# Kernel tuning notes

Hardware: AMD Instinct MI355X
Metric: run time of the kernel (lower is better)

Reference implementation:

```python
import jax, jax.numpy as jnp
import numpy as np

NEG = -10000.0
SLOPE = 0.2


def setup_inputs() -> dict:
    key = jax.random.key(0)
    k1, k2, k3, k4, k5 = jax.random.split(key, 5)
    B, N, F_in, F_out = 8, 2048, 512, 512
    text = jax.random.normal(k1, (B, N, F_in), dtype=jnp.float32)
    adj = jax.random.randint(k2, (B, N, N), 0, 2, dtype=jnp.int32)
    sc = 1.0 / np.sqrt(F_in)
    W = jax.random.normal(k3, (F_in, F_out), dtype=jnp.float32) * sc
    b = jnp.zeros((F_out,), dtype=jnp.float32)
    a_src = jax.random.normal(k4, (F_out,), dtype=jnp.float32) * sc
    a_dst = jax.random.normal(k5, (F_out,), dtype=jnp.float32) * sc
    return {"text": text, "adj": adj, "W": W, "b": b, "a_src": a_src, "a_dst": a_dst}


def reference(text, adj, W, b, a_src, a_dst):
    # hidden: [B, N, F_out]
    hidden = jnp.einsum("bnf,fo->bno", text, W) + b
    s = jnp.einsum("bno,o->bn", hidden, a_src)  # src score per node
    d = jnp.einsum("bno,o->bn", hidden, a_dst)  # dst score per node
    scores = s[:, :, None] + d[:, None, :]      # [B, N, N]
    scores = jnp.where(scores >= 0, scores, SLOPE * scores)  # LeakyReLU
    # faithful to original: masked_fill where adj.bool() is True
    scores = jnp.where(adj.astype(bool), NEG, scores)
    attn = jax.nn.softmax(scores, axis=-1)
    return jnp.einsum("bnm,bmo->bno", attn, hidden)
```

## Files before the change

kernel.cpp:

```cpp
#include <hip/hip_runtime.h>
#include <stdint.h>

#define NB 8
#define NN 2048
#define NF 512
#define TOTN (NB * NN)

typedef unsigned short u16;
typedef short bf16x8 __attribute__((ext_vector_type(8)));
typedef float f32x4 __attribute__((ext_vector_type(4)));

__device__ __forceinline__ u16 f2bf(float x) {
  unsigned u = __float_as_uint(x);
  unsigned r = 0x7FFFu + ((u >> 16) & 1u);
  return (u16)((u + r) >> 16);
}
__device__ __forceinline__ float bf2f(u16 u) {
  return __uint_as_float(((unsigned)u) << 16);
}

__device__ __forceinline__ void gl2lds16(const void* g, void* l) {
  __builtin_amdgcn_global_load_lds((const __attribute__((address_space(1))) void*)g,
                                   (__attribute__((address_space(3))) void*)l,
                                   16, 0, 0);
}

__global__ __launch_bounds__(256) void conv_kernel(
    const float* __restrict__ text, const float* __restrict__ W,
    u16* __restrict__ text_bf, u16* __restrict__ Wt) {
  int blk = blockIdx.x;
  if (blk < 8192) {
    int idx = blk * 256 + threadIdx.x;
    float4 v = ((const float4*)text)[idx];
    ushort4 o;
    o.x = f2bf(v.x); o.y = f2bf(v.y); o.z = f2bf(v.z); o.w = f2bf(v.w);
    ((ushort4*)text_bf)[idx] = o;
  } else {
    int t = (blk - 8192) * 256 + threadIdx.x;
    int o = t >> 9, f = t & 511;
    Wt[o * NF + f] = f2bf(W[f * NF + o]);
  }
}

template <int MODE>
__global__ __launch_bounds__(256) void gemm_kernel(
    const u16* __restrict__ A, int lda, size_t aOffPerZ,
    const u16* __restrict__ Bt, int ldb, size_t bOffPerZ,
    int K, const float* __restrict__ vec, void* __restrict__ Cptr) {
  __shared__ u16 Alds[128 * 32];
  __shared__ u16 Blds[128 * 32];

  const int z = blockIdx.z;
  const u16* Ab = A + aOffPerZ * (size_t)z;
  const u16* Bb = Bt + bOffPerZ * (size_t)z;
  const int bn = blockIdx.x, bm = blockIdx.y;
  const int t = threadIdx.x, wave = t >> 6, lane = t & 63;
  const int wm = (wave >> 1) * 64, wn = (wave & 1) * 64;

  f32x4 acc[4][4];
#pragma unroll
  for (int i = 0; i < 4; ++i)
#pragma unroll
    for (int j = 0; j < 4; ++j) acc[i][j] = (f32x4){0.f, 0.f, 0.f, 0.f};

  const int rowA0 = bm * 128, rowB0 = bn * 128;
  const int srow = (lane >> 2);
  const int scol = (lane & 3) * 8;

  for (int kt = 0; kt < K; kt += 32) {
#pragma unroll
    for (int q = 0; q < 2; ++q) {
      int r = wave * 32 + q * 16;
      gl2lds16(Ab + (size_t)(rowA0 + r + srow) * lda + (kt + scol),
               &Alds[r * 32]);
    }
#pragma unroll
    for (int q = 0; q < 2; ++q) {
      int r = wave * 32 + q * 16;
      gl2lds16(Bb + (size_t)(rowB0 + r + srow) * ldb + (kt + scol),
               &Blds[r * 32]);
    }
    __syncthreads();

    const int fr = lane & 15;
    const int k0 = (lane >> 4) * 8;
    bf16x8 af[4], bfr[4];
#pragma unroll
    for (int i = 0; i < 4; ++i)
      af[i] = *(const bf16x8*)&Alds[(wm + i * 16 + fr) * 32 + k0];
#pragma unroll
    for (int j = 0; j < 4; ++j)
      bfr[j] = *(const bf16x8*)&Blds[(wn + j * 16 + fr) * 32 + k0];
#pragma unroll
    for (int i = 0; i < 4; ++i)
#pragma unroll
      for (int j = 0; j < 4; ++j)
        acc[i][j] = __builtin_amdgcn_mfma_f32_16x16x32_bf16(af[i], bfr[j],
                                                            acc[i][j], 0, 0, 0);
    __syncthreads();
  }

  const int quad = lane >> 4, ln16 = lane & 15;
  if (MODE == 0) {
    u16* hT = (u16*)Cptr;
#pragma unroll
    for (int i = 0; i < 4; ++i) {
      int m0 = bm * 128 + wm + i * 16 + quad * 4;
#pragma unroll
      for (int r = 0; r < 4; ++r) {
        int m = m0 + r;
        float bias = vec[m];
#pragma unroll
        for (int j = 0; j < 4; ++j) {
          int n = bn * 128 + wn + j * 16 + ln16;
          hT[(size_t)m * TOTN + n] = f2bf(acc[i][j][r] + bias);
        }
      }
    }
  } else {
    float* outp = (float*)Cptr;
#pragma unroll
    for (int i = 0; i < 4; ++i) {
      int m0 = bm * 128 + wm + i * 16 + quad * 4;
#pragma unroll
      for (int r = 0; r < 4; ++r) {
        int m = m0 + r;
        float sc = vec[z * NN + m];
        size_t base = ((size_t)z * NN + m) * (size_t)NF;
#pragma unroll
        for (int j = 0; j < 4; ++j) {
          int n = bn * 128 + wn + j * 16 + ln16;
          outp[base + n] = acc[i][j][r] * sc;
        }
      }
    }
  }
}

__global__ __launch_bounds__(256) void sd_kernel(
    const u16* __restrict__ hT, const float* __restrict__ a_src,
    const float* __restrict__ a_dst, float* __restrict__ s,
    float* __restrict__ d) {
  int n = blockIdx.x * 256 + threadIdx.x;
  float as = 0.f, ad = 0.f;
#pragma unroll 8
  for (int o = 0; o < NF; ++o) {
    float h = bf2f(hT[(size_t)o * TOTN + n]);
    as = fmaf(h, a_src[o], as);
    ad = fmaf(h, a_dst[o], ad);
  }
  s[n] = as;
  d[n] = ad;
}

__global__ __launch_bounds__(256) void pmat_kernel(
    const int* __restrict__ adj, const float* __restrict__ s,
    const float* __restrict__ d, u16* __restrict__ P,
    float* __restrict__ linv) {
  int row = blockIdx.x;
  int b = row >> 11;
  float si = s[row];
  const int* arow = adj + (size_t)row * NN;
  const float* db = d + b * NN;
  u16* prow = P + (size_t)row * NN;
  int t = threadIdx.x;

  float lsum = 0.f;
#pragma unroll
  for (int c = 0; c < 2; ++c) {
    int j4 = c * 1024 + t * 4;
    int4 a4 = *(const int4*)&arow[j4];
    float4 d4 = *(const float4*)&db[j4];
    float x0 = si + d4.x, x1 = si + d4.y, x2 = si + d4.z, x3 = si + d4.w;
    x0 = fmaxf(x0, 0.2f * x0); x1 = fmaxf(x1, 0.2f * x1);
    x2 = fmaxf(x2, 0.2f * x2); x3 = fmaxf(x3, 0.2f * x3);
    float p0 = a4.x ? 0.f : __expf(x0);
    float p1 = a4.y ? 0.f : __expf(x1);
    float p2 = a4.z ? 0.f : __expf(x2);
    float p3 = a4.w ? 0.f : __expf(x3);
    lsum += (p0 + p1) + (p2 + p3);
    ushort4 pk;
    pk.x = f2bf(p0); pk.y = f2bf(p1); pk.z = f2bf(p2); pk.w = f2bf(p3);
    *(ushort4*)&prow[j4] = pk;
  }
#pragma unroll
  for (int off = 32; off > 0; off >>= 1) lsum += __shfl_down(lsum, off, 64);
  __shared__ float wsum[4];
  int wv = t >> 6, ln = t & 63;
  if (ln == 0) wsum[wv] = lsum;
  __syncthreads();
  if (t == 0) {
    float tot = wsum[0] + wsum[1] + wsum[2] + wsum[3];
    linv[row] = 1.0f / tot;
  }
}

extern "C" void kernel_launch(void* const* d_in, const int* in_sizes, int n_in,
                              void* d_out, int out_size, void* d_ws,
                              size_t ws_size, hipStream_t stream) {
  const float* text  = (const float*)d_in[0];
  const int*   adj   = (const int*)d_in[1];
  const float* W     = (const float*)d_in[2];
  const float* bias  = (const float*)d_in[3];
  const float* a_src = (const float*)d_in[4];
  const float* a_dst = (const float*)d_in[5];
  float* out = (float*)d_out;

  char* ws = (char*)d_ws;
  u16*   text_bf = (u16*)(ws + 0);
  u16*   Wt      = (u16*)(ws + 16777216);
  u16*   hT      = (u16*)(ws + 17301504);
  float* s       = (float*)(ws + 34078720);
  float* d       = (float*)(ws + 34144256);
  float* linv    = (float*)(ws + 34209792);
  u16*   P       = (u16*)(ws + 34275328);

  conv_kernel<<<9216, 256, 0, stream>>>(text, W, text_bf, Wt);

  gemm_kernel<0><<<dim3(128, 4, 1), 256, 0, stream>>>(
      Wt, NF, 0, text_bf, NF, 0, NF, bias, (void*)hT);

  sd_kernel<<<TOTN / 256, 256, 0, stream>>>(hT, a_src, a_dst, s, d);

  pmat_kernel<<<TOTN, 256, 0, stream>>>(adj, s, d, P, linv);

  gemm_kernel<1><<<dim3(4, 16, NB), 256, 0, stream>>>(
      P, NN, (size_t)NN * NN, hT, TOTN, (size_t)NN, NN, linv, (void*)out);
}
```

Baseline: 337.6 us.

## Fuse softmax probability generation into attention GEMM, drop P matrix round-trip

Builds the attention probability tile for 64 rows directly in LDS inside the second GEMM, so the bf16 P matrix is never written to or read from global memory, and the 1/rowsum scale is applied in the epilogue. Each block now covers the full 512-wide output with 8 waves. The sd kernel is also split across 4 threads per node with an LDS reduction to raise parallelism. The cost is that the exp work is repeated per k-step in a tighter loop with no prefetch overlap, the grid is smaller (256 blocks), and LDS use per block is larger.

After: 347.9 us. +3.0%, slower.

```diff
diff --git a/kernel.cpp b/kernel.cpp
--- a/kernel.cpp
+++ b/kernel.cpp
@@ -42,17 +42,13 @@
   }
 }
 
-template <int MODE>
-__global__ __launch_bounds__(256) void gemm_kernel(
-    const u16* __restrict__ A, int lda, size_t aOffPerZ,
-    const u16* __restrict__ Bt, int ldb, size_t bOffPerZ,
-    int K, const float* __restrict__ vec, void* __restrict__ Cptr) {
+__global__ __launch_bounds__(256) void gemm1_kernel(
+    const u16* __restrict__ A,
+    const u16* __restrict__ Bt,
+    const float* __restrict__ bias, u16* __restrict__ hT) {
   __shared__ u16 Alds[128 * 32];
   __shared__ u16 Blds[128 * 32];
 
-  const int z = blockIdx.z;
-  const u16* Ab = A + aOffPerZ * (size_t)z;
-  const u16* Bb = Bt + bOffPerZ * (size_t)z;
   const int bn = blockIdx.x, bm = blockIdx.y;
   const int t = threadIdx.x, wave = t >> 6, lane = t & 63;
   const int wm = (wave >> 1) * 64, wn = (wave & 1) * 64;
@@ -67,18 +63,16 @@
   const int srow = (lane >> 2);
   const int scol = (lane & 3) * 8;
 
-  for (int kt = 0; kt < K; kt += 32) {
+  for (int kt = 0; kt < NF; kt += 32) {
 #pragma unroll
     for (int q = 0; q < 2; ++q) {
       int r = wave * 32 + q * 16;
-      gl2lds16(Ab + (size_t)(rowA0 + r + srow) * lda + (kt + scol),
-               &Alds[r * 32]);
+      gl2lds16(A + (size_t)(rowA0 + r + srow) * NF + (kt + scol), &Alds[r * 32]);
     }
 #pragma unroll
     for (int q = 0; q < 2; ++q) {
       int r = wave * 32 + q * 16;
-      gl2lds16(Bb + (size_t)(rowB0 + r + srow) * ldb + (kt + scol),
-               &Blds[r * 32]);
+      gl2lds16(Bt + (size_t)(rowB0 + r + srow) * NF + (kt + scol), &Blds[r * 32]);
     }
     __syncthreads();
 
@@ -101,37 +95,17 @@
   }
 
   const int quad = lane >> 4, ln16 = lane & 15;
-  if (MODE == 0) {
-    u16* hT = (u16*)Cptr;
-#pragma unroll
-    for (int i = 0; i < 4; ++i) {
-      int m0 = bm * 128 + wm + i * 16 + quad * 4;
-#pragma unroll
-      for (int r = 0; r < 4; ++r) {
-        int m = m0 + r;
-        float bias = vec[m];
-#pragma unroll
-        for (int j = 0; j < 4; ++j) {
-          int n = bn * 128 + wn + j * 16 + ln16;
-          hT[(size_t)m * TOTN + n] = f2bf(acc[i][j][r] + bias);
-        }
-      }
-    }
-  } else {
-    float* outp = (float*)Cptr;
-#pragma unroll
-    for (int i = 0; i < 4; ++i) {
-      int m0 = bm * 128 + wm + i * 16 + quad * 4;
-#pragma unroll
-      for (int r = 0; r < 4; ++r) {
-        int m = m0 + r;
-        float sc = vec[z * NN + m];
-        size_t base = ((size_t)z * NN + m) * (size_t)NF;
-#pragma unroll
-        for (int j = 0; j < 4; ++j) {
-          int n = bn * 128 + wn + j * 16 + ln16;
-          outp[base + n] = acc[i][j][r] * sc;
-        }
+#pragma unroll
+  for (int i = 0; i < 4; ++i) {
+    int m0 = bm * 128 + wm + i * 16 + quad * 4;
+#pragma unroll
+    for (int r = 0; r < 4; ++r) {
+      int m = m0 + r;
+      float bv = bias[m];
+#pragma unroll
+      for (int j = 0; j < 4; ++j) {
+        int n = bn * 128 + wn + j * 16 + ln16;
+        hT[(size_t)m * TOTN + n] = f2bf(acc[i][j][r] + bv);
       }
     }
   }
@@ -141,36 +115,62 @@
     const u16* __restrict__ hT, const float* __restrict__ a_src,
     const float* __restrict__ a_dst, float* __restrict__ s,
     float* __restrict__ d) {
-  int n = blockIdx.x * 256 + threadIdx.x;
+  __shared__ float red[2][256];
+  int nb = blockIdx.x * 64;
+  int nl = threadIdx.x & 63;
+  int oo = threadIdx.x >> 6;
+  int n = nb + nl;
   float as = 0.f, ad = 0.f;
-#pragma unroll 8
-  for (int o = 0; o < NF; ++o) {
+#pragma unroll 4
+  for (int o = oo; o < NF; o += 4) {
     float h = bf2f(hT[(size_t)o * TOTN + n]);
     as = fmaf(h, a_src[o], as);
     ad = fmaf(h, a_dst[o], ad);
   }
-  s[n] = as;
-  d[n] = ad;
-}
-
-__global__ __launch_bounds__(256) void pmat_kernel(
+  red[0][threadIdx.x] = as;
+  red[1][threadIdx.x] = ad;
+  __syncthreads();
+  if (threadIdx.x < 64) {
+    int tt = threadIdx.x;
+    s[nb + tt] = red[0][tt] + red[0][tt + 64] + red[0][tt + 128] + red[0][tt + 192];
+    d[nb + tt] = red[1][tt] + red[1][tt + 64] + red[1][tt + 128] + red[1][tt + 192];
+  }
+}
+
+__global__ __launch_bounds__(512, 2) void fused_attn_kernel(
     const int* __restrict__ adj, const float* __restrict__ s,
-    const float* __restrict__ d, u16* __restrict__ P,
-    float* __restrict__ linv) {
-  int row = blockIdx.x;
-  int b = row >> 11;
-  float si = s[row];
-  const int* arow = adj + (size_t)row * NN;
-  const float* db = d + b * NN;
-  u16* prow = P + (size_t)row * NN;
-  int t = threadIdx.x;
+    const float* __restrict__ d, const u16* __restrict__ hT,
+    float* __restrict__ out) {
+  __shared__ u16 Plds[64 * 32];
+  __shared__ u16 Blds[512 * 32];
+  __shared__ float lpart[64 * 8];
+  __shared__ float linv_lds[64];
+
+  const int z = blockIdx.y;
+  const int i0 = blockIdx.x * 64;
+  const int t = threadIdx.x, wave = t >> 6, lane = t & 63;
+
+  const int pr = t >> 3;
+  const int pj = (t & 7) * 4;
+  const float si = s[z * NN + i0 + pr];
+  const int* arow = adj + (size_t)(z * NN + i0 + pr) * NN;
+  const float* db = d + z * NN;
+
+  const int so = wave * 16 + (lane >> 2);
+  const int sc = (lane & 3) * 8;
+
+  f32x4 acc[4][4];
+#pragma unroll
+  for (int i = 0; i < 4; ++i)
+#pragma unroll
+    for (int j = 0; j < 4; ++j) acc[i][j] = (f32x4){0.f, 0.f, 0.f, 0.f};
 
   float lsum = 0.f;
-#pragma unroll
-  for (int c = 0; c < 2; ++c) {
-    int j4 = c * 1024 + t * 4;
-    int4 a4 = *(const int4*)&arow[j4];
-    float4 d4 = *(const float4*)&db[j4];
+  const int ln16 = lane & 15, quad = lane >> 4;
+
+  for (int kt = 0; kt < NN; kt += 32) {
+    int4 a4 = *(const int4*)&arow[kt + pj];
+    float4 d4 = *(const float4*)&db[kt + pj];
     float x0 = si + d4.x, x1 = si + d4.y, x2 = si + d4.z, x3 = si + d4.w;
     x0 = fmaxf(x0, 0.2f * x0); x1 = fmaxf(x1, 0.2f * x1);
     x2 = fmaxf(x2, 0.2f * x2); x3 = fmaxf(x3, 0.2f * x3);
@@ -181,17 +181,56 @@
     lsum += (p0 + p1) + (p2 + p3);
     ushort4 pk;
     pk.x = f2bf(p0); pk.y = f2bf(p1); pk.z = f2bf(p2); pk.w = f2bf(p3);
-    *(ushort4*)&prow[j4] = pk;
-  }
-#pragma unroll
-  for (int off = 32; off > 0; off >>= 1) lsum += __shfl_down(lsum, off, 64);
-  __shared__ float wsum[4];
-  int wv = t >> 6, ln = t & 63;
-  if (ln == 0) wsum[wv] = lsum;
+    *(ushort4*)&Plds[pr * 32 + pj] = pk;
+
+#pragma unroll
+    for (int q = 0; q < 4; ++q) {
+      int ob = q * 128 + so;
+      gl2lds16(hT + (size_t)ob * TOTN + z * NN + kt + sc,
+               &Blds[(q * 128 + wave * 16) * 32]);
+    }
+    __syncthreads();
+
+    bf16x8 af[4], bfr[4];
+#pragma unroll
+    for (int i = 0; i < 4; ++i)
+      af[i] = *(const bf16x8*)&Plds[(i * 16 + ln16) * 32 + quad * 8];
+#pragma unroll
+    for (int j = 0; j < 4; ++j)
+      bfr[j] = *(const bf16x8*)&Blds[(wave * 64 + j * 16 + ln16) * 32 + quad * 8];
+#pragma unroll
+    for (int i = 0; i < 4; ++i)
+#pragma unroll
+      for (int j = 0; j < 4; ++j)
+        acc[i][j] = __builtin_amdgcn_mfma_f32_16x16x32_bf16(af[i], bfr[j],
+                                                            acc[i][j], 0, 0, 0);
+    __syncthreads();
+  }
+
+  lpart[pr * 8 + (t & 7)] = lsum;
   __syncthreads();
-  if (t == 0) {
-    float tot = wsum[0] + wsum[1] + wsum[2] + wsum[3];
-    linv[row] = 1.0f / tot;
+  if (t < 64) {
+    const float* lp = &lpart[t * 8];
+    float tot = ((lp[0] + lp[1]) + (lp[2] + lp[3])) +
+                ((lp[4] + lp[5]) + (lp[6] + lp[7]));
+    linv_lds[t] = 1.0f / tot;
+  }
+  __syncthreads();
+
+#pragma unroll
+  for (int i = 0; i < 4; ++i) {
+    int m0 = i * 16 + quad * 4;
+#pragma unroll
+    for (int r = 0; r < 4; ++r) {
+      int m = m0 + r;
+      float sc2 = linv_lds[m];
+      size_t base = (size_t)(z * NN + i0 + m) * NF;
+#pragma unroll
+      for (int j = 0; j < 4; ++j) {
+        int o = wave * 64 + j * 16 + ln16;
+        out[base + o] = acc[i][j][r] * sc2;
+      }
+    }
   }
 }
 
@@ -212,18 +251,12 @@
   u16*   hT      = (u16*)(ws + 17301504);
   float* s       = (float*)(ws + 34078720);
   float* d       = (float*)(ws + 34144256);
-  float* linv    = (float*)(ws + 34209792);
-  u16*   P       = (u16*)(ws + 34275328);
 
   conv_kernel<<<9216, 256, 0, stream>>>(text, W, text_bf, Wt);
 
-  gemm_kernel<0><<<dim3(128, 4, 1), 256, 0, stream>>>(
-      Wt, NF, 0, text_bf, NF, 0, NF, bias, (void*)hT);
-
-  sd_kernel<<<TOTN / 256, 256, 0, stream>>>(hT, a_src, a_dst, s, d);
-
-  pmat_kernel<<<TOTN, 256, 0, stream>>>(adj, s, d, P, linv);
-
-  gemm_kernel<1><<<dim3(4, 16, NB), 256, 0, stream>>>(
-      P, NN, (size_t)NN * NN, hT, TOTN, (size_t)NN, NN, linv, (void*)out);
-}
+  gemm1_kernel<<<dim3(128, 4, 1), 256, 0, stream>>>(Wt, text_bf, bias, hT);
+
+  sd_kernel<<<TOTN / 64, 256, 0, stream>>>(hT, a_src, a_dst, s, d);
+
+  fused_attn_kernel<<<dim3(NN / 64, NB, 1), 512, 0, stream>>>(adj, s, d, hT, out);
+}
```
